# Optimization experiments

Measured on AMD Instinct MI355X. Metric: run time of the kernel, lower is better.

The kernel has to match this reference:

```python
import jax, jax.numpy as jnp
import numpy as np
import math

DIM = 1024
SEQ = 2048
BATCH = 4
LN_EPS = 1e-5


def _linear_params(key, fan_in, fan_out):
    # torch nn.Linear default init: U(-1/sqrt(fan_in), 1/sqrt(fan_in))
    k1, k2 = jax.random.split(key)
    bound = 1.0 / math.sqrt(fan_in)
    W = jax.random.uniform(k1, (fan_out, fan_in), minval=-bound, maxval=bound, dtype=jnp.float32)
    b = jax.random.uniform(k2, (fan_out,), minval=-bound, maxval=bound, dtype=jnp.float32)
    return W, b


def setup_inputs() -> dict:
    key = jax.random.key(0)
    ks = jax.random.split(key, 9)
    x = jax.random.normal(ks[0], (BATCH, SEQ, DIM), dtype=jnp.float32)
    base_phases = jax.random.normal(ks[1], (SEQ, DIM), dtype=jnp.float32) * math.pi
    Wk, bk = _linear_params(ks[2], DIM, DIM)
    Wv, bv = _linear_params(ks[3], DIM, DIM)
    Wq, bq = _linear_params(ks[4], DIM, DIM)
    Wkm, bkm = _linear_params(ks[5], DIM, DIM)
    Wqm, bqm = _linear_params(ks[6], DIM, DIM)
    Wo, bo = _linear_params(ks[7], DIM, DIM)
    mod_scale = jnp.ones((1,), dtype=jnp.float32) * 0.1
    ln_g = jnp.ones((DIM,), dtype=jnp.float32)
    ln_b = jnp.zeros((DIM,), dtype=jnp.float32)
    return dict(x=x, base_phases=base_phases, Wk=Wk, bk=bk, Wv=Wv, bv=bv,
                Wq=Wq, bq=bq, Wkm=Wkm, bkm=bkm, Wqm=Wqm, bqm=bqm,
                mod_scale=mod_scale, ln_g=ln_g, ln_b=ln_b, Wo=Wo, bo=bo)


def _lin(x, W, b):
    return jnp.einsum('bsd,ed->bse', x, W) + b


def reference(x, base_phases, Wk, bk, Wv, bv, Wq, bq, Wkm, bkm, Wqm, bqm,
              mod_scale, ln_g, ln_b, Wo, bo):
    dim = x.shape[-1]
    base_phase = base_phases[None, :, :]  # [1, S, D]
    key = _lin(x, Wk, bk)
    value = _lin(x, Wv, bv)
    query = _lin(x, Wq, bq)
    key_phase = base_phase + _lin(key, Wkm, bkm) * mod_scale
    query_phase = base_phase + _lin(query, Wqm, bqm) * mod_scale
    # bind value with complex phasor exp(i*key_phase), prefix-sum over seq
    mem_real = jnp.cumsum(value * jnp.cos(key_phase), axis=1)
    mem_imag = jnp.cumsum(value * jnp.sin(key_phase), axis=1)
    # phase-matched retrieval: Re(mem * exp(-i*query_phase))
    retrieved = (mem_real * jnp.cos(query_phase) + mem_imag * jnp.sin(query_phase))
    retrieved = retrieved / math.sqrt(dim)
    # LayerNorm then output projection
    mu = jnp.mean(retrieved, axis=-1, keepdims=True)
    var = jnp.var(retrieved, axis=-1, keepdims=True)
    normed = (retrieved - mu) * jax.lax.rsqrt(var + LN_EPS) * ln_g + ln_b
    out = _lin(normed, Wo, bo)
    return x + out
```

## Files before the change

### kernel.cpp

```cpp
#include <hip/hip_runtime.h>
#include <math.h>

#define DIM 1024
#define SEQ 2048
#define BATCH 4
#define ROWS (BATCH*SEQ)
#define CHUNKS 128
#define CLEN (SEQ/CHUNKS)
#define N3 3072
#define LN_EPS 1e-5f
#define NTK 16

typedef unsigned short ushort_t;
typedef __attribute__((ext_vector_type(8))) short bf16x8;
typedef __attribute__((ext_vector_type(4))) float f32x4;

static const size_t NE = (size_t)ROWS * DIM;
static const size_t WN = (size_t)DIM * DIM;

__device__ inline ushort_t f2bf(float f) {
    union { float f; unsigned u; } v; v.f = f;
    unsigned r = v.u + 0x7FFFu + ((v.u >> 16) & 1u);
    return (ushort_t)(r >> 16);
}
__device__ inline float bf2f(ushort_t u) { return __uint_as_float((unsigned)u << 16); }
__device__ inline float bf_lo(unsigned p) { return __uint_as_float(p << 16); }
__device__ inline float bf_hi(unsigned p) { return __uint_as_float(p & 0xFFFF0000u); }
__device__ inline float bfq(float f) { return bf2f(f2bf(f)); }

__global__ __launch_bounds__(256)
void conv_all_k(const float* __restrict__ x,  const float* __restrict__ Wv,
                const float* __restrict__ Wo, const float* __restrict__ Wkm,
                const float* __restrict__ Wqm,
                ushort_t* __restrict__ xbf,   ushort_t* __restrict__ W3,
                ushort_t* __restrict__ wo_b,  ushort_t* __restrict__ wkm_b,
                ushort_t* __restrict__ wqm_b)
{
    size_t e = ((size_t)blockIdx.x * 256 + threadIdx.x) * 8;
    const float* src; ushort_t* dst; size_t off;
    if      (e < NE)          { src = x;   dst = xbf;   off = e; }
    else if (e < NE + WN)     { src = Wv;  dst = W3;    off = e - NE; }
    else if (e < NE + 2*WN)   { src = Wo;  dst = wo_b;  off = e - NE - 2*WN + WN; }
    else if (e < NE + 3*WN)   { src = Wkm; dst = wkm_b; off = e - NE - 2*WN; }
    else                      { src = Wqm; dst = wqm_b; off = e - NE - 3*WN; }
    float4 a = *(const float4*)(src + off);
    float4 b = *(const float4*)(src + off + 4);
    ushort4 lo, hi;
    lo.x = f2bf(a.x); lo.y = f2bf(a.y); lo.z = f2bf(a.z); lo.w = f2bf(a.w);
    hi.x = f2bf(b.x); hi.y = f2bf(b.y); hi.z = f2bf(b.z); hi.w = f2bf(b.w);
    *(ushort4*)(dst + off) = lo;
    *(ushort4*)(dst + off + 4) = hi;
}

__global__ __launch_bounds__(256)
void transpose2_k(const float* __restrict__ Wk, const float* __restrict__ Wq,
                  ushort_t* __restrict__ wkT, ushort_t* __restrict__ wqT)
{
    const float* in = blockIdx.z ? Wq : Wk;
    ushort_t* out   = blockIdx.z ? wqT : wkT;
    __shared__ ushort_t tile[32][33];
    const int bx = blockIdx.x, by = blockIdx.y;
    const int tx = threadIdx.x & 31, ty = threadIdx.x >> 5;
    #pragma unroll
    for (int j = 0; j < 4; ++j) {
        int r = by * 32 + ty + j * 8;
        tile[ty + j * 8][tx] = f2bf(in[(size_t)r * DIM + bx * 32 + tx]);
    }
    __syncthreads();
    #pragma unroll
    for (int j = 0; j < 4; ++j) {
        int r = bx * 32 + ty + j * 8;
        out[(size_t)r * DIM + by * 32 + tx] = tile[tx][ty + j * 8];
    }
}

__global__ __launch_bounds__(256)
void matvec2_k(const float* __restrict__ Wkm, const float* __restrict__ bk,
               const float* __restrict__ bkm, float* __restrict__ bck,
               const float* __restrict__ Wqm, const float* __restrict__ bq,
               const float* __restrict__ bqm, float* __restrict__ bcq)
{
    int z = blockIdx.y;
    const float* Wm  = z ? Wqm : Wkm;
    const float* bi  = z ? bq  : bk;
    const float* bo_ = z ? bqm : bkm;
    float* bc        = z ? bcq : bck;
    int e = blockIdx.x * 4 + (threadIdx.x >> 6);
    int l = threadIdx.x & 63;
    float s = 0.f;
    #pragma unroll
    for (int j = 0; j < DIM / 64; ++j)
        s += Wm[(size_t)e * DIM + l + j * 64] * bi[l + j * 64];
    #pragma unroll
    for (int o = 32; o >= 1; o >>= 1) s += __shfl_down(s, o);
    if (l == 0) bc[e] = s + bo_[e];
}

__global__ __launch_bounds__(256)
void gemm_combine2(const ushort_t* __restrict__ A0, const ushort_t* __restrict__ W0,
                   ushort_t* __restrict__ C0,
                   const ushort_t* __restrict__ A1, const ushort_t* __restrict__ W1,
                   ushort_t* __restrict__ C1)
{
    const ushort_t* A = blockIdx.z ? A1 : A0;
    const ushort_t* W = blockIdx.z ? W1 : W0;
    ushort_t*       C = blockIdx.z ? C1 : C0;
    __shared__ ushort_t As[128 * 32];
    __shared__ ushort_t Bs[128 * 32];
    const int bm = blockIdx.x * 128;
    const int bn = blockIdx.y * 128;
    const int t = threadIdx.x;
    const int lane = t & 63;
    const int w = t >> 6, wr = w >> 1, wc = w & 1;
    f32x4 acc[4][4] = {};
    const int fr = lane & 15;
    const int kc = (lane >> 4) * 8;
    for (int k0 = 0; k0 < DIM; k0 += 32) {
        #pragma unroll
        for (int i = 0; i < 2; ++i) {
            int c = t + i * 256;
            int row = c >> 2;
            int col = (c & 3) * 8;
            const ushort_t* ga = A + (size_t)(bm + row) * DIM + k0 + col;
            __builtin_amdgcn_global_load_lds(
                (const __attribute__((address_space(1))) void*)ga,
                (__attribute__((address_space(3))) void*)(As + (size_t)c * 8), 16, 0, 0);
            const ushort_t* gb = W + (size_t)(bn + row) * DIM + k0 + col;
            __builtin_amdgcn_global_load_lds(
                (const __attribute__((address_space(1))) void*)gb,
                (__attribute__((address_space(3))) void*)(Bs + (size_t)c * 8), 16, 0, 0);
        }
        __syncthreads();
        bf16x8 af[4], bw[4];
        #pragma unroll
        for (int m2 = 0; m2 < 4; ++m2)
            af[m2] = *(const bf16x8*)(As + (wr * 64 + m2 * 16 + fr) * 32 + kc);
        #pragma unroll
        for (int n2 = 0; n2 < 4; ++n2)
            bw[n2] = *(const bf16x8*)(Bs + (wc * 64 + n2 * 16 + fr) * 32 + kc);
        #pragma unroll
        for (int m2 = 0; m2 < 4; ++m2)
            #pragma unroll
            for (int n2 = 0; n2 < 4; ++n2)
                acc[m2][n2] = __builtin_amdgcn_mfma_f32_16x16x32_bf16(
                    af[m2], bw[n2], acc[m2][n2], 0, 0, 0);
        __syncthreads();
    }
    const int fc = lane & 15;
    const int r0 = (lane >> 4) * 4;
    #pragma unroll
    for (int m2 = 0; m2 < 4; ++m2)
        #pragma unroll
        for (int n2 = 0; n2 < 4; ++n2) {
            int col = bn + wc * 64 + n2 * 16 + fc;
            #pragma unroll
            for (int r = 0; r < 4; ++r) {
                int row = bm + wr * 64 + m2 * 16 + r0 + r;
                C[(size_t)row * DIM + col] = f2bf(acc[m2][n2][r]);
            }
        }
}

template<int MODE, int BN>
__global__ __launch_bounds__(512)
void gemm_pipe(const ushort_t* __restrict__ A, const ushort_t* __restrict__ W,
               const float* __restrict__ bias, const float* __restrict__ resid,
               void* __restrict__ Cout, int N)
{
    constexpr int NF   = BN / 64;
    constexpr int BUFU = (2048 + BN * 8) * 8;
    __shared__ __align__(16) ushort_t lds[2 * BUFU];

    const int nwg  = gridDim.x * gridDim.y;
    const int orig = blockIdx.y * gridDim.x + blockIdx.x;
    const int swz  = (orig & 7) * (nwg >> 3) + (orig >> 3);
    const int bm   = (swz & 31) * 256;
    const int bn   = (swz >> 5) * BN;

    const int t = threadIdx.x;
    const int lane = t & 63;
    const int w = t >> 6;
    const int wr = w >> 2;
    const int wc = w & 3;
    const int fr = lane & 15;
    const int hi = lane >> 4;

    f32x4 acc[8][NF] = {};

    auto SA = [&](int kt, ushort_t* buf, int i) {
        int c = t + i * 512;
        int row = c >> 3, ls = c & 7, gs = ls ^ (row & 7);
        const ushort_t* g = A + (size_t)(bm + row) * 1024 + kt * 64 + gs * 8;
        __builtin_amdgcn_global_load_lds(
            (const __attribute__((address_space(1))) void*)g,
            (__attribute__((address_space(3))) void*)(buf + (size_t)c * 8), 16, 0, 0);
    };
    auto SB = [&](int kt, ushort_t* buf, int i) {
        int c = t + i * 512;
        int row = c >> 3, ls = c & 7, gs = ls ^ (row & 7);
        const ushort_t* g = W + (size_t)(bn + row) * 1024 + kt * 64 + gs * 8;
        __builtin_amdgcn_global_load_lds(
            (const __attribute__((address_space(1))) void*)g,
            (__attribute__((address_space(3))) void*)(buf + 16384 + (size_t)c * 8), 16, 0, 0);
    };

    #pragma unroll
    for (int i = 0; i < 4; ++i) SA(0, lds, i);
    #pragma unroll
    for (int i = 0; i < NF; ++i) SB(0, lds, i);

    for (int tt = 0; tt < NTK; ++tt) {
        ushort_t* cur = lds + (tt & 1) * BUFU;
        ushort_t* nxt = lds + ((tt + 1) & 1) * BUFU;
        const bool st = (tt + 1 < NTK);
        asm volatile("s_waitcnt vmcnt(0)\n\ts_barrier" ::: "memory");

        const ushort_t* As = cur;
        const ushort_t* Bs = cur + 16384;
        bf16x8 bw[NF][2];
        #pragma unroll
        for (int n2 = 0; n2 < NF; ++n2)
            #pragma unroll
            for (int kk = 0; kk < 2; ++kk) {
                int row = wc * (BN / 4) + n2 * 16 + fr;
                bw[n2][kk] = *(const bf16x8*)(Bs + row * 64 + ((kk * 4 + hi) ^ (row & 7)) * 8);
            }
        #pragma unroll
        for (int p = 0; p < 4; ++p) {
            bf16x8 af[2][2];
            #pragma unroll
            for (int j = 0; j < 2; ++j)
                #pragma unroll
                for (int kk = 0; kk < 2; ++kk) {
                    int row = wr * 128 + (p * 2 + j) * 16 + fr;
                    af[j][kk] = *(const bf16x8*)(As + row * 64 + ((kk * 4 + hi) ^ (row & 7)) * 8);
                }
            if (st) {
                if      (p == 0) { SA(tt + 1, nxt, 0); SA(tt + 1, nxt, 1); }
                else if (p == 1) { SA(tt + 1, nxt, 2); SA(tt + 1, nxt, 3); }
                else if (p == 2) { SB(tt + 1, nxt, 0); if (NF > 1) SB(tt + 1, nxt, 1); }
                else             { if (NF > 2) SB(tt + 1, nxt, 2); }
            }
            __builtin_amdgcn_s_barrier();
            asm volatile("s_waitcnt lgkmcnt(0)" ::: "memory");
            __builtin_amdgcn_sched_barrier(0);
            __builtin_amdgcn_s_setprio(1);
            #pragma unroll
            for (int j = 0; j < 2; ++j)
                #pragma unroll
                for (int n2 = 0; n2 < NF; ++n2)
                    #pragma unroll
                    for (int kk = 0; kk < 2; ++kk)
                        acc[p * 2 + j][n2] = __builtin_amdgcn_mfma_f32_16x16x32_bf16(
                            af[j][kk], bw[n2][kk], acc[p * 2 + j][n2], 0, 0, 0);
            __builtin_amdgcn_s_setprio(0);
        }
    }

    const int fc = fr;
    const int r0 = hi * 4;
    #pragma unroll
    for (int m2 = 0; m2 < 8; ++m2)
        #pragma unroll
        for (int n2 = 0; n2 < NF; ++n2) {
            int col = bn + wc * (BN / 4) + n2 * 16 + fc;
            float bv;
            if (MODE == 6) bv = (col < 1024) ? bias[col] : 0.0f;
            else           bv = bias[col];
            #pragma unroll
            for (int r = 0; r < 4; ++r) {
                int row = bm + wr * 128 + m2 * 16 + r0 + r;
                size_t idx = (size_t)row * N + col;
                float v = acc[m2][n2][r] + bv;
                if (MODE == 4) ((float*)Cout)[idx] = v + resid[idx];
                else           ((ushort_t*)Cout)[idx] = f2bf(v);
            }
        }
}

__global__ __launch_bounds__(256)
void phase_scan1_k(const ushort_t* __restrict__ act3, const float* __restrict__ bp,
                   const float* __restrict__ bck, const float* __restrict__ ms_p,
                   unsigned* __restrict__ ab,
                   float* __restrict__ sumr, float* __restrict__ sumi)
{
    const int blk = blockIdx.x;
    const int b = blk >> 7;
    const int c = blk & (CHUNKS - 1);
    const int d0 = threadIdx.x * 4;
    const float ms = ms_p[0];
    const float4 bc4 = *(const float4*)(bck + d0);
    float sr0 = 0.f, sr1 = 0.f, sr2 = 0.f, sr3 = 0.f;
    float si0 = 0.f, si1 = 0.f, si2 = 0.f, si3 = 0.f;
    const size_t row0 = (size_t)b * SEQ + (size_t)c * CLEN;

    #pragma unroll 2
    for (int s = 0; s < CLEN; ++s) {
        size_t row = row0 + s;
        ushort4 v4 = *(const ushort4*)(act3 + row * N3 + d0);
        ushort4 k4 = *(const ushort4*)(act3 + row * N3 + 1024 + d0);
        float4 bp4 = *(const float4*)(bp + ((size_t)(c * CLEN + s)) * DIM + d0);
        uint4 o;
        float vv, kp, sn, cs, ar, ai;
        vv = bf2f(v4.x); kp = bp4.x + (bf2f(k4.x) + bc4.x) * ms;
        sincosf(kp, &sn, &cs); ar = bfq(vv * cs); ai = bfq(vv * sn);
        sr0 += ar; si0 += ai;
        o.x = (unsigned)f2bf(ar) | ((unsigned)f2bf(ai) << 16);
        vv = bf2f(v4.y); kp = bp4.y + (bf2f(k4.y) + bc4.y) * ms;
        sincosf(kp, &sn, &cs); ar = bfq(vv * cs); ai = bfq(vv * sn);
        sr1 += ar; si1 += ai;
        o.y = (unsigned)f2bf(ar) | ((unsigned)f2bf(ai) << 16);
        vv = bf2f(v4.z); kp = bp4.z + (bf2f(k4.z) + bc4.z) * ms;
        sincosf(kp, &sn, &cs); ar = bfq(vv * cs); ai = bfq(vv * sn);
        sr2 += ar; si2 += ai;
        o.z = (unsigned)f2bf(ar) | ((unsigned)f2bf(ai) << 16);
        vv = bf2f(v4.w); kp = bp4.w + (bf2f(k4.w) + bc4.w) * ms;
        sincosf(kp, &sn, &cs); ar = bfq(vv * cs); ai = bfq(vv * sn);
        sr3 += ar; si3 += ai;
        o.w = (unsigned)f2bf(ar) | ((unsigned)f2bf(ai) << 16);
        *(uint4*)(ab + row * DIM + d0) = o;
    }
    int sgid = (b * CHUNKS + c) * DIM + d0;
    *(float4*)(sumr + sgid) = make_float4(sr0, sr1, sr2, sr3);
    *(float4*)(sumi + sgid) = make_float4(si0, si1, si2, si3);
}

__global__ __launch_bounds__(256)
void scan_pass2(float* __restrict__ sumr, float* __restrict__ sumi)
{
    int wid  = (blockIdx.x * 256 + threadIdx.x) >> 6;
    int lane = threadIdx.x & 63;
    int b = wid >> 10;
    int d = wid & (DIM - 1);
    int i0 = (b * CHUNKS + 2 * lane) * DIM + d;
    int i1 = i0 + DIM;
    float r0 = sumr[i0], r1 = sumr[i1];
    float s0 = sumi[i0], s1 = sumi[i1];
    float pr = r0 + r1, pi = s0 + s1;
    float er = pr, ei = pi;
    #pragma unroll
    for (int o = 1; o < 64; o <<= 1) {
        float tr = __shfl_up(er, o);
        float ti = __shfl_up(ei, o);
        if (lane >= o) { er += tr; ei += ti; }
    }
    er -= pr; ei -= pi;
    sumr[i0] = er;       sumi[i0] = ei;
    sumr[i1] = er + r0;  sumi[i1] = ei + s0;
}

__global__ __launch_bounds__(256)
void scan3_ln_k(const unsigned* __restrict__ ab, const ushort_t* __restrict__ act3,
                const float* __restrict__ bp, const float* __restrict__ bcq,
                const float* __restrict__ ms_p,
                const float* __restrict__ sumr, const float* __restrict__ sumi,
                const float* __restrict__ g, const float* __restrict__ beta,
                ushort_t* __restrict__ normbf)
{
    const int blk = blockIdx.x;
    const int b = blk >> 7;
    const int c = blk & (CHUNKS - 1);
    const int t = threadIdx.x;
    const int d0 = t * 4;
    const float ms = ms_p[0];
    const float4 bq4 = *(const float4*)(bcq + d0);
    const float4 gv  = *(const float4*)(g + d0);
    const float4 btv = *(const float4*)(beta + d0);
    const float inv_sqrt_dim = 0.03125f;

    int sgid = (b * CHUNKS + c) * DIM + d0;
    float4 rrv = *(const float4*)(sumr + sgid);
    float4 riv = *(const float4*)(sumi + sgid);
    float rr0 = rrv.x, rr1 = rrv.y, rr2 = rrv.z, rr3 = rrv.w;
    float ri0 = riv.x, ri1 = riv.y, ri2 = riv.z, ri3 = riv.w;

    const size_t row0 = (size_t)b * SEQ + (size_t)c * CLEN;
    __shared__ float red[16];
    const int wv = t >> 6, lane = t & 63;

    uint4   abv = *(const uint4*)(ab + row0 * DIM + d0);
    ushort4 q4  = *(const ushort4*)(act3 + row0 * N3 + 2048 + d0);
    float4  bp4 = *(const float4*)(bp + (size_t)(c * CLEN) * DIM + d0);

    for (int s = 0; s < CLEN; ++s) {
        uint4 abc = abv; ushort4 qc = q4; float4 bpc = bp4;
        if (s + 1 < CLEN) {
            size_t row = row0 + s + 1;
            abv = *(const uint4*)(ab + row * DIM + d0);
            q4  = *(const ushort4*)(act3 + row * N3 + 2048 + d0);
            bp4 = *(const float4*)(bp + (size_t)(c * CLEN + s + 1) * DIM + d0);
        }
        float r0g, r1g, r2g, r3g, qp, sq, cq;
        rr0 += bf_lo(abc.x); ri0 += bf_hi(abc.x);
        qp = bpc.x + (bf2f(qc.x) + bq4.x) * ms; sincosf(qp, &sq, &cq);
        r0g = (rr0 * cq + ri0 * sq) * inv_sqrt_dim;
        rr1 += bf_lo(abc.y); ri1 += bf_hi(abc.y);
        qp = bpc.y + (bf2f(qc.y) + bq4.y) * ms; sincosf(qp, &sq, &cq);
        r1g = (rr1 * cq + ri1 * sq) * inv_sqrt_dim;
        rr2 += bf_lo(abc.z); ri2 += bf_hi(abc.z);
        qp = bpc.z + (bf2f(qc.z) + bq4.z) * ms; sincosf(qp, &sq, &cq);
        r2g = (rr2 * cq + ri2 * sq) * inv_sqrt_dim;
        rr3 += bf_lo(abc.w); ri3 += bf_hi(abc.w);
        qp = bpc.w + (bf2f(qc.w) + bq4.w) * ms; sincosf(qp, &sq, &cq);
        r3g = (rr3 * cq + ri3 * sq) * inv_sqrt_dim;

        float ssum = r0g + r1g + r2g + r3g;
        float ssq  = r0g*r0g + r1g*r1g + r2g*r2g + r3g*r3g;
        #pragma unroll
        for (int o = 32; o >= 1; o >>= 1) {
            ssum += __shfl_down(ssum, o);
            ssq  += __shfl_down(ssq, o);
        }
        float* rd = red + (s & 1) * 8;
        if (lane == 0) { rd[wv] = ssum; rd[wv + 4] = ssq; }
        __syncthreads();
        if (t == 0) {
            rd[0] = rd[0] + rd[1] + rd[2] + rd[3];
            rd[4] = rd[4] + rd[5] + rd[6] + rd[7];
        }
        __syncthreads();
        float mu  = rd[0] * (1.0f / DIM);
        float var = rd[4] * (1.0f / DIM) - mu * mu;
        float rstd = rsqrtf(var + LN_EPS);
        ushort4 o;
        o.x = f2bf((r0g - mu) * rstd * gv.x + btv.x);
        o.y = f2bf((r1g - mu) * rstd * gv.y + btv.y);
        o.z = f2bf((r2g - mu) * rstd * gv.z + btv.z);
        o.w = f2bf((r3g - mu) * rstd * gv.w + btv.w);
        *(ushort4*)(normbf + (row0 + s) * DIM + d0) = o;
    }
}

extern "C" void kernel_launch(void* const* d_in, const int* in_sizes, int n_in,
                              void* d_out, int out_size, void* d_ws, size_t ws_size,
                              hipStream_t stream)
{
    const float* x   = (const float*)d_in[0];
    const float* bp  = (const float*)d_in[1];
    const float* Wk  = (const float*)d_in[2];
    const float* bk  = (const float*)d_in[3];
    const float* Wv  = (const float*)d_in[4];
    const float* bv  = (const float*)d_in[5];
    const float* Wq  = (const float*)d_in[6];
    const float* bq  = (const float*)d_in[7];
    const float* Wkm = (const float*)d_in[8];
    const float* bkm = (const float*)d_in[9];
    const float* Wqm = (const float*)d_in[10];
    const float* bqm = (const float*)d_in[11];
    const float* ms  = (const float*)d_in[12];
    const float* lng = (const float*)d_in[13];
    const float* lnb = (const float*)d_in[14];
    const float* Wo  = (const float*)d_in[15];
    const float* bo  = (const float*)d_in[16];
    float* out = (float*)d_out;

    unsigned* ab     = (unsigned*)d_ws;
    ushort_t* act3   = (ushort_t*)(ab + NE);
    ushort_t* xbf    = act3 + (size_t)ROWS * N3;
    ushort_t* normbf = xbf + NE;
    ushort_t* W3     = normbf + NE;
    ushort_t* wo_b   = W3 + (size_t)N3 * DIM;
    ushort_t* wkm_b  = wo_b + WN;
    ushort_t* wqm_b  = wkm_b + WN;
    ushort_t* wkT_b  = wqm_b + WN;
    ushort_t* wqT_b  = wkT_b + WN;
    float* bck       = (float*)(wqT_b + WN);
    float* bcq       = bck + DIM;
    float* sumr      = bcq + DIM;
    float* sumi      = sumr + (size_t)BATCH * CHUNKS * DIM;

    conv_all_k<<<(int)((NE + 4 * WN) / 2048), 256, 0, stream>>>(
        x, Wv, Wo, Wkm, Wqm, xbf, W3, wo_b, wkm_b, wqm_b);
    dim3 tg(32, 32, 2);
    transpose2_k<<<tg, 256, 0, stream>>>(Wk, Wq, wkT_b, wqT_b);
    dim3 mg(DIM / 4, 2);
    matvec2_k<<<mg, 256, 0, stream>>>(Wkm, bk, bkm, bck, Wqm, bq, bqm, bcq);
    dim3 gw(DIM / 128, DIM / 128, 2);
    gemm_combine2<<<gw, 256, 0, stream>>>(wkm_b, wkT_b, W3 + WN,
                                          wqm_b, wqT_b, W3 + 2 * WN);

    dim3 g3(32, N3 / 192);
    gemm_pipe<6, 192><<<g3, 512, 0, stream>>>(xbf, W3, bv, nullptr, act3, N3);

    phase_scan1_k<<<BATCH * CHUNKS, 256, 0, stream>>>(act3, bp, bck, ms,
                                                      ab, sumr, sumi);
    scan_pass2<<<(BATCH * DIM) / 4, 256, 0, stream>>>(sumr, sumi);
    scan3_ln_k<<<BATCH * CHUNKS, 256, 0, stream>>>(ab, act3, bp, bcq, ms,
                                                   sumr, sumi, lng, lnb, normbf);

    dim3 gg(32, DIM / 128);
    gemm_pipe<4, 128><<<gg, 512, 0, stream>>>(normbf, wo_b, bo, x, out, DIM);
}
```

Measured before the change: 202.8 us.

## Split GEMM K-tile into half-tiles with finer vmcnt pipelining and wider N tile

Restructures the bf16 MFMA GEMM so each 64-wide K tile is staged as two 32-wide halves with a new XOR swizzle. Partial vmcnt waits let compute on the first half start while the second half is still in flight. It also removes the workgroup index swizzle in favour of direct block mapping, and widens the QKV-fused GEMM tile from 192 to 256 columns. The wider tile raises register and LDS use and cuts workgroup count (12 vs 16 column blocks), which may reduce occupancy and change L2 locality.

After: 193.2 us. 4.7% less time.

```diff
diff --git a/kernel.cpp b/kernel.cpp
--- a/kernel.cpp
+++ b/kernel.cpp
@@ -168,15 +168,11 @@
                void* __restrict__ Cout, int N)
 {
     constexpr int NF   = BN / 64;
-    constexpr int BUFU = (2048 + BN * 8) * 8;
+    constexpr int BUFU = 16384 + BN * 64;
     __shared__ __align__(16) ushort_t lds[2 * BUFU];
 
-    const int nwg  = gridDim.x * gridDim.y;
-    const int orig = blockIdx.y * gridDim.x + blockIdx.x;
-    const int swz  = (orig & 7) * (nwg >> 3) + (orig >> 3);
-    const int bm   = (swz & 31) * 256;
-    const int bn   = (swz >> 5) * BN;
-
+    const int bm = blockIdx.x * 256;
+    const int bn = blockIdx.y * BN;
     const int t = threadIdx.x;
     const int lane = t & 63;
     const int w = t >> 6;
@@ -187,75 +183,92 @@
 
     f32x4 acc[8][NF] = {};
 
-    auto SA = [&](int kt, ushort_t* buf, int i) {
-        int c = t + i * 512;
-        int row = c >> 3, ls = c & 7, gs = ls ^ (row & 7);
-        const ushort_t* g = A + (size_t)(bm + row) * 1024 + kt * 64 + gs * 8;
-        __builtin_amdgcn_global_load_lds(
-            (const __attribute__((address_space(1))) void*)g,
-            (__attribute__((address_space(3))) void*)(buf + (size_t)c * 8), 16, 0, 0);
+    auto SA = [&](int kt, ushort_t* buf, int h) {
+        #pragma unroll
+        for (int i = 0; i < 2; ++i) {
+            int c = t + i * 512;
+            int row = c >> 2, sl = c & 3, sg = sl ^ ((row >> 1) & 3);
+            const ushort_t* g = A + (size_t)(bm + row) * 1024 + kt * 64 + h * 32 + sg * 8;
+            __builtin_amdgcn_global_load_lds(
+                (const __attribute__((address_space(1))) void*)g,
+                (__attribute__((address_space(3))) void*)(buf + h * 8192 + (size_t)c * 8),
+                16, 0, 0);
+        }
     };
-    auto SB = [&](int kt, ushort_t* buf, int i) {
-        int c = t + i * 512;
-        int row = c >> 3, ls = c & 7, gs = ls ^ (row & 7);
-        const ushort_t* g = W + (size_t)(bn + row) * 1024 + kt * 64 + gs * 8;
-        __builtin_amdgcn_global_load_lds(
-            (const __attribute__((address_space(1))) void*)g,
-            (__attribute__((address_space(3))) void*)(buf + 16384 + (size_t)c * 8), 16, 0, 0);
+    auto SB = [&](int kt, ushort_t* buf, int h) {
+        #pragma unroll
+        for (int i = 0; i < BN / 128; ++i) {
+            int c = t + i * 512;
+            int row = c >> 2, sl = c & 3, sg = sl ^ ((row >> 1) & 3);
+            const ushort_t* g = W + (size_t)(bn + row) * 1024 + kt * 64 + h * 32 + sg * 8;
+            __builtin_amdgcn_global_load_lds(
+                (const __attribute__((address_space(1))) void*)g,
+                (__attribute__((address_space(3))) void*)(buf + 16384 + h * (BN * 32) + (size_t)c * 8),
+                16, 0, 0);
+        }
     };
 
-    #pragma unroll
-    for (int i = 0; i < 4; ++i) SA(0, lds, i);
-    #pragma unroll
-    for (int i = 0; i < NF; ++i) SB(0, lds, i);
+#define GPHASE(KK, MH, STAGE_STMT)                                           \
+    {                                                                        \
+        bf16x8 af[4];                                                        \
+        _Pragma("unroll")                                                    \
+        for (int j = 0; j < 4; ++j) {                                        \
+            int row = wr * 128 + ((MH) * 4 + j) * 16 + fr;                   \
+            af[j] = *(const bf16x8*)(As + (KK) * 8192 + row * 32 +           \
+                                     (hi ^ ((row >> 1) & 3)) * 8);           \
+        }                                                                    \
+        if ((MH) == 0) {                                                     \
+            _Pragma("unroll")                                                \
+            for (int nf = 0; nf < NF; ++nf) {                                \
+                int row = wc * (BN / 4) + nf * 16 + fr;                      \
+                bw[nf] = *(const bf16x8*)(Bs + (KK) * (BN * 32) + row * 32 + \
+                                          (hi ^ ((row >> 1) & 3)) * 8);      \
+            }                                                                \
+        }                                                                    \
+        STAGE_STMT;                                                          \
+        __builtin_amdgcn_s_barrier();                                        \
+        asm volatile("s_waitcnt lgkmcnt(0)" ::: "memory");                   \
+        __builtin_amdgcn_sched_barrier(0);                                   \
+        __builtin_amdgcn_s_setprio(1);                                       \
+        _Pragma("unroll")                                                    \
+        for (int j = 0; j < 4; ++j)                                          \
+            _Pragma("unroll")                                                \
+            for (int nf = 0; nf < NF; ++nf)                                  \
+                acc[(MH) * 4 + j][nf] = __builtin_amdgcn_mfma_f32_16x16x32_bf16( \
+                    af[j], bw[nf], acc[(MH) * 4 + j][nf], 0, 0, 0);          \
+        __builtin_amdgcn_s_setprio(0);                                       \
+        __builtin_amdgcn_s_barrier();                                        \
+    }
+
+    SA(0, lds, 0); SB(0, lds, 0); SA(0, lds, 1); SB(0, lds, 1);
 
     for (int tt = 0; tt < NTK; ++tt) {
-        ushort_t* cur = lds + (tt & 1) * BUFU;
-        ushort_t* nxt = lds + ((tt + 1) & 1) * BUFU;
+        ushort_t* base = lds + (tt & 1) * BUFU;
+        ushort_t* nbuf = lds + ((tt + 1) & 1) * BUFU;
+        const ushort_t* As = base;
+        const ushort_t* Bs = base + 16384;
         const bool st = (tt + 1 < NTK);
-        asm volatile("s_waitcnt vmcnt(0)\n\ts_barrier" ::: "memory");
-
-        const ushort_t* As = cur;
-        const ushort_t* Bs = cur + 16384;
-        bf16x8 bw[NF][2];
-        #pragma unroll
-        for (int n2 = 0; n2 < NF; ++n2)
-            #pragma unroll
-            for (int kk = 0; kk < 2; ++kk) {
-                int row = wc * (BN / 4) + n2 * 16 + fr;
-                bw[n2][kk] = *(const bf16x8*)(Bs + row * 64 + ((kk * 4 + hi) ^ (row & 7)) * 8);
-            }
-        #pragma unroll
-        for (int p = 0; p < 4; ++p) {
-            bf16x8 af[2][2];
-            #pragma unroll
-            for (int j = 0; j < 2; ++j)
-                #pragma unroll
-                for (int kk = 0; kk < 2; ++kk) {
-                    int row = wr * 128 + (p * 2 + j) * 16 + fr;
-                    af[j][kk] = *(const bf16x8*)(As + row * 64 + ((kk * 4 + hi) ^ (row & 7)) * 8);
-                }
-            if (st) {
-                if      (p == 0) { SA(tt + 1, nxt, 0); SA(tt + 1, nxt, 1); }
-                else if (p == 1) { SA(tt + 1, nxt, 2); SA(tt + 1, nxt, 3); }
-                else if (p == 2) { SB(tt + 1, nxt, 0); if (NF > 1) SB(tt + 1, nxt, 1); }
-                else             { if (NF > 2) SB(tt + 1, nxt, 2); }
-            }
-            __builtin_amdgcn_s_barrier();
-            asm volatile("s_waitcnt lgkmcnt(0)" ::: "memory");
-            __builtin_amdgcn_sched_barrier(0);
-            __builtin_amdgcn_s_setprio(1);
-            #pragma unroll
-            for (int j = 0; j < 2; ++j)
-                #pragma unroll
-                for (int n2 = 0; n2 < NF; ++n2)
-                    #pragma unroll
-                    for (int kk = 0; kk < 2; ++kk)
-                        acc[p * 2 + j][n2] = __builtin_amdgcn_mfma_f32_16x16x32_bf16(
-                            af[j][kk], bw[n2][kk], acc[p * 2 + j][n2], 0, 0, 0);
-            __builtin_amdgcn_s_setprio(0);
-        }
-    }
+        bf16x8 bw[NF];
+
+        if constexpr (NF == 4) asm volatile("s_waitcnt vmcnt(4)" ::: "memory");
+        else                   asm volatile("s_waitcnt vmcnt(3)" ::: "memory");
+        __builtin_amdgcn_s_barrier();
+
+        GPHASE(0, 0, if (st) SA(tt + 1, nbuf, 0));
+        GPHASE(0, 1, if (st) SB(tt + 1, nbuf, 0));
+
+        if (st) {
+            if constexpr (NF == 4) asm volatile("s_waitcnt vmcnt(4)" ::: "memory");
+            else                   asm volatile("s_waitcnt vmcnt(3)" ::: "memory");
+        } else {
+            asm volatile("s_waitcnt vmcnt(0)" ::: "memory");
+        }
+        __builtin_amdgcn_s_barrier();
+
+        GPHASE(1, 0, if (st) SA(tt + 1, nbuf, 1));
+        GPHASE(1, 1, if (st) SB(tt + 1, nbuf, 1));
+    }
+#undef GPHASE
 
     const int fc = fr;
     const int r0 = hi * 4;
@@ -479,8 +492,8 @@
     gemm_combine2<<<gw, 256, 0, stream>>>(wkm_b, wkT_b, W3 + WN,
                                           wqm_b, wqT_b, W3 + 2 * WN);
 
-    dim3 g3(32, N3 / 192);
-    gemm_pipe<6, 192><<<g3, 512, 0, stream>>>(xbf, W3, bv, nullptr, act3, N3);
+    dim3 g3(32, N3 / 256);
+    gemm_pipe<6, 256><<<g3, 512, 0, stream>>>(xbf, W3, bv, nullptr, act3, N3);
 
     phase_scan1_k<<<BATCH * CHUNKS, 256, 0, stream>>>(act3, bp, bck, ms,
                                                       ab, sumr, sumi);
```
